# Performance work log

Hardware: AMD Instinct MI355X
Metric: run time of the kernel (lower is better)

## Reference

```python
import jax, jax.numpy as jnp
import numpy as np
import math

E = 512; V = 8192; B = 32; T = 16; L = 4; FF = 2048; NH = 8; TEMP = 1.0


def setup_inputs() -> dict:
    key = jax.random.key(0)
    ks = jax.random.split(key, 16)
    s = 0.02
    nrm = lambda k, shape, sc=s: jax.random.normal(k, shape, jnp.float32) * sc
    d = {}
    d['encoder_state'] = nrm(ks[0], (1, B, E), 1.0)
    d['special_symbol'] = nrm(ks[1], (1, 1, E))
    d['embed_weight'] = nrm(ks[2], (V, E), E ** -0.5)
    d['out_w'] = nrm(ks[3], (V, E))
    d['out_b'] = jnp.zeros((V,), jnp.float32)
    u = jax.random.uniform(ks[4], (T, B, V), jnp.float32, 1e-6, 1.0 - 1e-6)
    d['gumbel'] = -jnp.log(-jnp.log(u))
    d['sa_qkv_w'] = nrm(ks[5], (L, 3 * E, E)); d['sa_qkv_b'] = jnp.zeros((L, 3 * E), jnp.float32)
    d['sa_out_w'] = nrm(ks[6], (L, E, E)); d['sa_out_b'] = jnp.zeros((L, E), jnp.float32)
    d['ca_qkv_w'] = nrm(ks[7], (L, 3 * E, E)); d['ca_qkv_b'] = jnp.zeros((L, 3 * E), jnp.float32)
    d['ca_out_w'] = nrm(ks[8], (L, E, E)); d['ca_out_b'] = jnp.zeros((L, E), jnp.float32)
    for i in (1, 2, 3):
        d['ln%d_g' % i] = jnp.ones((L, E), jnp.float32)
        d['ln%d_b' % i] = jnp.zeros((L, E), jnp.float32)
    d['w1'] = nrm(ks[9], (L, FF, E)); d['b1'] = jnp.zeros((L, FF), jnp.float32)
    d['w2'] = nrm(ks[10], (L, E, FF)); d['b2'] = jnp.zeros((L, E), jnp.float32)
    return d


def _ln(x, g, b):
    m = x.mean(-1, keepdims=True)
    v = ((x - m) ** 2).mean(-1, keepdims=True)
    return (x - m) / jnp.sqrt(v + 1e-5) * g + b


def _mha(q_in, kv_in, qkv_w, qkv_b, out_w, out_b, mask):
    # q_in: [Sq,B,E], kv_in: [Sk,B,E]; fused PyTorch-style in_proj
    hd = E // NH
    wq, wk, wv = jnp.split(qkv_w, 3, 0)
    bq, bk, bv = jnp.split(qkv_b, 3, 0)
    q = (q_in @ wq.T + bq).reshape(q_in.shape[0], -1, NH, hd)
    k = (kv_in @ wk.T + bk).reshape(kv_in.shape[0], -1, NH, hd)
    v = (kv_in @ wv.T + bv).reshape(kv_in.shape[0], -1, NH, hd)
    s = jnp.einsum('qbhd,kbhd->bhqk', q, k) / math.sqrt(hd)
    if mask is not None:
        s = s + mask
    a = jax.nn.softmax(s, -1)
    o = jnp.einsum('bhqk,kbhd->qbhd', a, v).reshape(q_in.shape[0], -1, E)
    return o @ out_w.T + out_b


def _forward(encoder_state, special_symbol, embed_weight, out_w, out_b, gumbel,
             sa_qkv_w, sa_qkv_b, sa_out_w, sa_out_b,
             ca_qkv_w, ca_qkv_b, ca_out_w, ca_out_b,
             ln1_g, ln1_b, ln2_g, ln2_b, ln3_g, ln3_b,
             w1, b1, w2, b2):
    bsz = encoder_state.shape[1]
    embed_scale = math.sqrt(E)
    inp = jnp.broadcast_to(special_symbol, (1, bsz, E))  # special start symbol
    seq_steps, distribs = [], []
    for step in range(T):
        t = step + 1
        mask = jnp.where(jnp.triu(jnp.ones((t, t), bool), 1), -jnp.inf, 0.0)
        x = inp
        for l in range(L):  # post-norm TransformerDecoderLayer, erf-gelu
            sa = _mha(x, x, sa_qkv_w[l], sa_qkv_b[l], sa_out_w[l], sa_out_b[l], mask)
            x = _ln(x + sa, ln1_g[l], ln1_b[l])
            ca = _mha(x, encoder_state, ca_qkv_w[l], ca_qkv_b[l], ca_out_w[l], ca_out_b[l], None)
            x = _ln(x + ca, ln2_g[l], ln2_b[l])
            ff = jax.nn.gelu(x @ w1[l].T + b1[l], approximate=False) @ w2[l].T + b2[l]
            x = _ln(x + ff, ln3_g[l], ln3_b[l])
        logits = x[-1] @ out_w.T + out_b  # [B,V], last position only
        distribs.append(jax.nn.softmax(logits, -1))
        sample = jax.nn.softmax((logits + gumbel[step]) / TEMP, -1)  # gumbel-softmax (training mode)
        seq_steps.append(sample)
        new_emb = (sample @ embed_weight) * embed_scale  # soft embedding lookup
        inp = jnp.concatenate([inp, new_emb[None]], 0)
    sequence = jnp.stack(seq_steps).transpose(1, 0, 2)  # [B,T,V]
    eos = jnp.zeros_like(sequence[:, :1, :]).at[:, :, 0].set(1.0)
    sequence = jnp.concatenate([sequence, eos], 1)  # [B,T+1,V]
    return sequence, jnp.stack(distribs)  # distribs: [T,B,V]


def reference(encoder_state, special_symbol, embed_weight, out_w, out_b, gumbel,
              sa_qkv_w, sa_qkv_b, sa_out_w, sa_out_b,
              ca_qkv_w, ca_qkv_b, ca_out_w, ca_out_b,
              ln1_g, ln1_b, ln2_g, ln2_b, ln3_g, ln3_b,
              w1, b1, w2, b2):
    return _forward(encoder_state, special_symbol, embed_weight, out_w, out_b, gumbel,
                    sa_qkv_w, sa_qkv_b, sa_out_w, sa_out_b,
                    ca_qkv_w, ca_qkv_b, ca_out_w, ca_out_b,
                    ln1_g, ln1_b, ln2_g, ln2_b, ln3_g, ln3_b,
                    w1, b1, w2, b2)
```

## Files before the change

kernel.cpp:

```cpp
#include <hip/hip_runtime.h>
#include <math.h>

#define BB 32
#define EE 512
#define VV 8192
#define TT 16
#define LL 4
#define FFD 2048
#define NHD 8
#define HDD 64
#define LDP 520
#define RWP 516
#define OLP 72
#define SCALE_EMB 22.627416997969522f

typedef __attribute__((ext_vector_type(8))) short bf16x8;
typedef __attribute__((ext_vector_type(4))) float f32x4;
typedef unsigned long long ull;

__device__ __forceinline__ f32x4 mfma16(bf16x8 a, bf16x8 b, f32x4 c){
  return __builtin_amdgcn_mfma_f32_16x16x32_bf16(a, b, c, 0, 0, 0);
}

__device__ __forceinline__ float wave_sum(float v){
  for (int o = 32; o; o >>= 1) v += __shfl_down(v, o);
  return __shfl(v, 0);
}
__device__ __forceinline__ unsigned short f_to_bf(float f){
  unsigned u = __float_as_uint(f);
  unsigned r = (u + 0x7fffu + ((u >> 16) & 1u)) >> 16;
  return (unsigned short)r;
}
__device__ __forceinline__ float2 bf2_to_f2(const unsigned short* p){
  unsigned u = *(const unsigned*)p;
  float2 r;
  r.x = __uint_as_float(u << 16);
  r.y = __uint_as_float(u & 0xffff0000u);
  return r;
}
union UF { ull u; unsigned short s[4]; };
__device__ __forceinline__ ull pkbf4(float a, float b, float c, float d){
  UF x; x.s[0] = f_to_bf(a); x.s[1] = f_to_bf(b); x.s[2] = f_to_bf(c); x.s[3] = f_to_bf(d); return x.u;
}

__device__ __forceinline__ void gemm_chunk(const float* __restrict__ wrow0, int ldw,
    const unsigned short* xs, float* wt, float acc[4][2]){
  const int t = threadIdx.x, fg = t & 15, bg = t >> 4;
  #pragma unroll 1
  for (int c = 0; c < 8; ++c){
    const int k0 = c*64;
    __syncthreads();
    {
      int i = t*4;
      #pragma unroll
      for (int p = 0; p < 4; ++p, i += 1024){
        const int fr = i >> 6, kk = i & 63;
        float4 v = *(const float4*)(wrow0 + (size_t)fr*ldw + k0 + kk);
        wt[(kk+0)*68 + fr] = v.x;
        wt[(kk+1)*68 + fr] = v.y;
        wt[(kk+2)*68 + fr] = v.z;
        wt[(kk+3)*68 + fr] = v.w;
      }
    }
    __syncthreads();
    const unsigned short* xr0 = xs + (bg*2)*EE + k0;
    const unsigned short* xr1 = xr0 + EE;
    #pragma unroll 8
    for (int k = 0; k < 64; k += 2){
      float w0[4], w1[4];
      *(float4*)w0 = *(const float4*)(wt + (k+0)*68 + fg*4);
      *(float4*)w1 = *(const float4*)(wt + (k+1)*68 + fg*4);
      float2 xv0 = bf2_to_f2(xr0 + k);
      float2 xv1 = bf2_to_f2(xr1 + k);
      #pragma unroll
      for (int i = 0; i < 4; ++i){
        acc[i][0] += w0[i]*xv0.x + w1[i]*xv0.y;
        acc[i][1] += w0[i]*xv1.x + w1[i]*xv1.y;
      }
    }
  }
}

__device__ __forceinline__ void stage_x_512(unsigned short* xs,
    const float* __restrict__ xraw, const float* __restrict__ ybuf,
    const float* __restrict__ g, const float* __restrict__ bt, int use_ln,
    float* __restrict__ xlnout){
  if (!use_ln){
    for (int i = threadIdx.x*4; i < BB*EE; i += 2048){
      float4 v = *(const float4*)(xraw + i);
      int r = i >> 9, c = i & 511;
      *(ull*)(xs + r*LDP + c) = pkbf4(v.x, v.y, v.z, v.w);
    }
  } else {
    const int lane = threadIdx.x & 63, wv = threadIdx.x >> 6;
    for (int r = wv*4; r < wv*4 + 4; ++r){
      float vals[8]; float s = 0.f, s2 = 0.f;
      #pragma unroll
      for (int j = 0; j < 8; ++j){
        float v = ybuf[r*EE + lane + j*64];
        vals[j] = v; s += v; s2 += v*v;
      }
      s = wave_sum(s); s2 = wave_sum(s2);
      float m = s * (1.f/EE);
      float inv = rsqrtf(s2*(1.f/EE) - m*m + 1e-5f);
      #pragma unroll
      for (int j = 0; j < 8; ++j){
        int c = lane + j*64;
        float v = (vals[j]-m)*inv*g[c] + bt[c];
        xs[r*LDP + c] = f_to_bf(v);
        if (xlnout) xlnout[r*EE + c] = v;
      }
    }
  }
  __syncthreads();
}


__global__ __launch_bounds__(256) void k_init(const float* __restrict__ special,
    float* __restrict__ dseq, float* __restrict__ x,
    float* __restrict__ o2a, float* __restrict__ o2b,
    float* __restrict__ y0, float* __restrict__ y1){
  int idx = blockIdx.x*256 + threadIdx.x;
  if (idx < BB*VV){
    int b = idx >> 13, v = idx & (VV-1);
    dseq[(size_t)b*((TT+1)*VV) + (size_t)TT*VV + v] = (v == 0) ? 1.f : 0.f;
  } else if (idx < BB*VV + BB*EE){
    x[idx - BB*VV] = special[idx & (EE-1)];
  } else if (idx < BB*VV + 2*BB*EE){
    o2a[idx - BB*VV - BB*EE] = 0.f;
  } else if (idx < BB*VV + 3*BB*EE){
    o2b[idx - BB*VV - 2*BB*EE] = 0.f;
  } else if (idx < BB*VV + 4*BB*EE){
    y0[idx - BB*VV - 3*BB*EE] = 0.f;
  } else if (idx < BB*VV + 5*BB*EE){
    y1[idx - BB*VV - 4*BB*EE] = 0.f;
  }
}

__global__ __launch_bounds__(256) void k_penc(const float* __restrict__ enc,
    const float* __restrict__ w, const float* __restrict__ bias, float* __restrict__ venc){
  __shared__ unsigned short xs[BB*EE];
  __shared__ float wt[64*68];
  const int l = blockIdx.x >> 3, et = blockIdx.x & 7;
  for (int i = threadIdx.x; i < BB*EE; i += 256) xs[i] = f_to_bf(enc[i]);
  const int t = threadIdx.x, fg = t & 15, bg = t >> 4;
  const int f0 = et*64;
  const float* wl = w + (size_t)l*3*EE*EE + (size_t)(2*EE + f0)*EE;
  const float* bl = bias + l*3*EE + 2*EE + f0;
  float acc[4][2];
  #pragma unroll
  for (int i = 0; i < 4; ++i){ float bv = bl[fg*4+i]; acc[i][0] = bv; acc[i][1] = bv; }
  gemm_chunk(wl, EE, xs, wt, acc);
  #pragma unroll
  for (int i = 0; i < 4; ++i)
    #pragma unroll
    for (int j = 0; j < 2; ++j)
      venc[(size_t)l*BB*EE + (bg*2+j)*EE + f0 + fg*4 + i] = acc[i][j];
}

__global__ __launch_bounds__(256) void k_pca(const float* __restrict__ venc,
    const float* __restrict__ w, const float* __restrict__ bias, float* __restrict__ cac){
  __shared__ unsigned short xs[BB*EE];
  __shared__ float wt[64*68];
  const int l = blockIdx.x >> 3, et = blockIdx.x & 7;
  const float* vin = venc + (size_t)l*BB*EE;
  for (int i = threadIdx.x; i < BB*EE; i += 256) xs[i] = f_to_bf(vin[i]);
  const int t = threadIdx.x, fg = t & 15, bg = t >> 4;
  const int f0 = et*64;
  const float* wl = w + (size_t)l*EE*EE + (size_t)f0*EE;
  const float* bl = bias + l*EE + f0;
  float acc[4][2];
  #pragma unroll
  for (int i = 0; i < 4; ++i){ float bv = bl[fg*4+i]; acc[i][0] = bv; acc[i][1] = bv; }
  gemm_chunk(wl, EE, xs, wt, acc);
  #pragma unroll
  for (int i = 0; i < 4; ++i)
    #pragma unroll
    for (int j = 0; j < 2; ++j)
      cac[(size_t)l*BB*EE + (bg*2+j)*EE + f0 + fg*4 + i] = acc[i][j];
}

__global__ __launch_bounds__(256) void k_cvt(const float* __restrict__ s,
    unsigned short* __restrict__ d, int n4){
  int i = blockIdx.x*256 + threadIdx.x;
  if (i < n4){
    float4 v = ((const float4*)s)[i];
    ushort4 o;
    o.x = f_to_bf(v.x); o.y = f_to_bf(v.y); o.z = f_to_bf(v.z); o.w = f_to_bf(v.w);
    ((ushort4*)d)[i] = o;
  }
}

__global__ __launch_bounds__(256) void k_embT(const float* __restrict__ emb,
    unsigned short* __restrict__ eT){
  __shared__ unsigned short tl[64][68];
  const int vt = blockIdx.x >> 3, et = blockIdx.x & 7;
  const int v0 = vt*64, e0 = et*64;
  for (int i = threadIdx.x; i < 64*64; i += 256){
    int vv = i >> 6, ee = i & 63;
    tl[vv][ee] = f_to_bf(emb[(size_t)(v0+vv)*EE + e0 + ee]);
  }
  __syncthreads();
  for (int i = threadIdx.x; i < 64*64; i += 256){
    int ee = i >> 6, vv = i & 63;
    eT[(size_t)(e0+ee)*VV + v0 + vv] = tl[vv][ee];
  }
}


__global__ __launch_bounds__(512) void k_A(
    const float* __restrict__ x, const float* __restrict__ ybuf,
    const float* __restrict__ lng, const float* __restrict__ lnb, int use_ln,
    const unsigned short* __restrict__ Wb, const float* __restrict__ bias,
    const unsigned short* __restrict__ owb_l,
    float* __restrict__ kcl, float* __restrict__ vcl,
    float* __restrict__ xln, float* __restrict__ o2,
    float* __restrict__ gs, int tpos, int tlen){
  __shared__ unsigned short xs[BB*LDP];
  __shared__ __align__(16) float qs[BB*68];
  __shared__ float att[BB*16];
  const int h = blockIdx.x;
  const int t = threadIdx.x;
  if (!use_ln && h == 0 && t < 64) gs[t] = 0.f;
  stage_x_512(xs, x, ybuf, lng, lnb, use_ln, (use_ln && h == 0) ? xln : nullptr);
  const int wv = t >> 6, lane = t & 63;
  const int lm = lane & 15, kg = lane >> 4;
  const unsigned short* b0r = xs + lm*LDP + kg*8;
  const unsigned short* b1r = xs + (lm+16)*LDP + kg*8;
  if (wv < 6){
    const int c = wv >> 1, half = wv & 1;
    #pragma unroll
    for (int ft = 0; ft < 2; ++ft){
      const int frel_t = (half*2 + ft)*16;
      const unsigned short* ar = Wb + (size_t)(c*EE + h*64 + frel_t + lm)*EE + kg*8;
      f32x4 acc0 = {0.f,0.f,0.f,0.f}, acc1 = {0.f,0.f,0.f,0.f};
      #pragma unroll 4
      for (int ks = 0; ks < 16; ++ks){
        bf16x8 a  = *reinterpret_cast<const bf16x8*>(ar + ks*32);
        bf16x8 b0 = *reinterpret_cast<const bf16x8*>(b0r + ks*32);
        bf16x8 b1 = *reinterpret_cast<const bf16x8*>(b1r + ks*32);
        acc0 = mfma16(a, b0, acc0);
        acc1 = mfma16(a, b1, acc1);
      }
      #pragma unroll
      for (int r = 0; r < 4; ++r){
        const int frel = frel_t + kg*4 + r;
        const float bv = bias[c*EE + h*64 + frel];
        float v0 = acc0[r] + bv, v1 = acc1[r] + bv;
        if (c == 0){
          qs[lm*68 + frel] = v0;
          qs[(lm+16)*68 + frel] = v1;
        } else if (c == 1){
          kcl[((lm*NHD + h)*TT + tpos)*HDD + frel] = v0;
          kcl[(((lm+16)*NHD + h)*TT + tpos)*HDD + frel] = v1;
        } else {
          vcl[((lm*NHD + h)*TT + tpos)*HDD + frel] = v0;
          vcl[(((lm+16)*NHD + h)*TT + tpos)*HDD + frel] = v1;
        }
      }
    }
  }
  __syncthreads();
  {
    const int b = t >> 4, j = t & 15;
    if (j < tlen){
      const float* qrow = qs + b*68;
      const float* krow = kcl + ((b*NHD + h)*TT + j)*HDD;
      float a = 0.f;
      #pragma unroll
      for (int d = 0; d < HDD; d += 4){
        float4 qv = *(const float4*)(qrow + d);
        float4 kv = *(const float4*)(krow + d);
        a += qv.x*kv.x + qv.y*kv.y + qv.z*kv.z + qv.w*kv.w;
      }
      att[b*16 + j] = a*0.125f;
    }
  }
  __syncthreads();
  if (t < 32){
    const int b = t;
    float m = -1e30f;
    for (int j = 0; j < tlen; ++j) m = fmaxf(m, att[b*16 + j]);
    float s = 0.f;
    for (int j = 0; j < tlen; ++j) s += __expf(att[b*16 + j] - m);
    float inv = 1.f/s;
    for (int j = 0; j < tlen; ++j) att[b*16 + j] = __expf(att[b*16 + j] - m)*inv;
  }
  __syncthreads();
  unsigned short* o_lds = (unsigned short*)qs;
  {
    const int b = t >> 4, d0 = (t & 15)*4;
    float acc[4];
    #pragma unroll
    for (int i = 0; i < 4; ++i) acc[i] = 0.f;
    const float* vrow = vcl + ((b*NHD + h)*TT)*HDD + d0;
    for (int j = 0; j < tlen; ++j){
      const float a = att[b*16 + j];
      float4 v = *(const float4*)(vrow + j*HDD);
      acc[0] += a*v.x; acc[1] += a*v.y; acc[2] += a*v.z; acc[3] += a*v.w;
    }
    *(ull*)(o_lds + b*OLP + d0) = pkbf4(acc[0], acc[1], acc[2], acc[3]);
  }
  __syncthreads();
  const unsigned short* ob0 = o_lds + lm*OLP + kg*8;
  const unsigned short* ob1 = o_lds + (lm+16)*OLP + kg*8;
  #pragma unroll
  for (int ft = 0; ft < 4; ++ft){
    const int f0 = wv*64 + ft*16;
    const unsigned short* ar = owb_l + (size_t)(f0 + lm)*EE + h*HDD + kg*8;
    f32x4 a0 = {0.f,0.f,0.f,0.f}, a1 = {0.f,0.f,0.f,0.f};
    #pragma unroll
    for (int ks = 0; ks < 2; ++ks){
      bf16x8 a  = *reinterpret_cast<const bf16x8*>(ar + ks*32);
      bf16x8 x0 = *reinterpret_cast<const bf16x8*>(ob0 + ks*32);
      bf16x8 x1 = *reinterpret_cast<const bf16x8*>(ob1 + ks*32);
      a0 = mfma16(a, x0, a0);
      a1 = mfma16(a, x1, a1);
    }
    #pragma unroll
    for (int r = 0; r < 4; ++r){
      const int f = f0 + kg*4 + r;
      atomicAdd(&o2[lm*EE + f], a0[r]);
      atomicAdd(&o2[(lm+16)*EE + f], a1[r]);
    }
  }
}

__global__ __launch_bounds__(512) void k_BC(
    const float* __restrict__ o2buf, const float* __restrict__ resid,
    const float* __restrict__ ob, const float* __restrict__ cac,
    const float* __restrict__ g1, const float* __restrict__ b1g,
    const float* __restrict__ g2, const float* __restrict__ b2g,
    const float* __restrict__ b2bias,
    const unsigned short* __restrict__ w1b, const float* __restrict__ b1bias,
    const unsigned short* __restrict__ w2b,
    float* __restrict__ ycur, float* __restrict__ yzero, float* __restrict__ o2zero,
    float* __restrict__ xz){
  __shared__ unsigned short xs[BB*LDP];
  __shared__ __align__(16) float rawf[BB*RWP];
  __shared__ unsigned short Hs[BB*OLP];
  const int t = threadIdx.x, blk = blockIdx.x;
  for (int i = t*4; i < BB*EE; i += 2048){
    const int r = i >> 9, c = i & 511;
    float4 a  = *(const float4*)(o2buf + i);
    float4 rr = *(const float4*)(resid + i);
    float4 ov = *(const float4*)(ob + c);
    rawf[r*RWP + c]     = a.x + rr.x + ov.x;
    rawf[r*RWP + c + 1] = a.y + rr.y + ov.y;
    rawf[r*RWP + c + 2] = a.z + rr.z + ov.z;
    rawf[r*RWP + c + 3] = a.w + rr.w + ov.w;
  }
  __syncthreads();
  const int wv = t >> 6, lane = t & 63;
  const int lm = lane & 15, kg = lane >> 4;
  {
    const int c0 = lane*4, c1 = 256 + lane*4;
    for (int r = wv*4; r < wv*4 + 4; ++r){
      float v[8];
      *(float4*)(v+0) = *(const float4*)(rawf + r*RWP + c0);
      *(float4*)(v+4) = *(const float4*)(rawf + r*RWP + c1);
      float s = 0.f, s2 = 0.f;
      #pragma unroll
      for (int j = 0; j < 8; ++j){ s += v[j]; s2 += v[j]*v[j]; }
      s = wave_sum(s); s2 = wave_sum(s2);
      float m = s*(1.f/EE), inv = rsqrtf(s2*(1.f/EE) - m*m + 1e-5f);
      float4 ca0 = *(const float4*)(cac + (size_t)r*EE + c0);
      float4 ca1 = *(const float4*)(cac + (size_t)r*EE + c1);
      float nv[8]; float u = 0.f, u2 = 0.f;
      nv[0] = (v[0]-m)*inv*g1[c0+0] + b1g[c0+0] + ca0.x;
      nv[1] = (v[1]-m)*inv*g1[c0+1] + b1g[c0+1] + ca0.y;
      nv[2] = (v[2]-m)*inv*g1[c0+2] + b1g[c0+2] + ca0.z;
      nv[3] = (v[3]-m)*inv*g1[c0+3] + b1g[c0+3] + ca0.w;
      nv[4] = (v[4]-m)*inv*g1[c1+0] + b1g[c1+0] + ca1.x;
      nv[5] = (v[5]-m)*inv*g1[c1+1] + b1g[c1+1] + ca1.y;
      nv[6] = (v[6]-m)*inv*g1[c1+2] + b1g[c1+2] + ca1.z;
      nv[7] = (v[7]-m)*inv*g1[c1+3] + b1g[c1+3] + ca1.w;
      #pragma unroll
      for (int j = 0; j < 8; ++j){ u += nv[j]; u2 += nv[j]*nv[j]; }
      u = wave_sum(u); u2 = wave_sum(u2);
      float m2 = u*(1.f/EE), inv2 = rsqrtf(u2*(1.f/EE) - m2*m2 + 1e-5f);
      float o0 = (nv[0]-m2)*inv2*g2[c0+0] + b2g[c0+0];
      float o1 = (nv[1]-m2)*inv2*g2[c0+1] + b2g[c0+1];
      float o2v = (nv[2]-m2)*inv2*g2[c0+2] + b2g[c0+2];
      float o3 = (nv[3]-m2)*inv2*g2[c0+3] + b2g[c0+3];
      float o4 = (nv[4]-m2)*inv2*g2[c1+0] + b2g[c1+0];
      float o5 = (nv[5]-m2)*inv2*g2[c1+1] + b2g[c1+1];
      float o6 = (nv[6]-m2)*inv2*g2[c1+2] + b2g[c1+2];
      float o7 = (nv[7]-m2)*inv2*g2[c1+3] + b2g[c1+3];
      *(ull*)(xs + r*LDP + c0) = pkbf4(o0, o1, o2v, o3);
      *(ull*)(xs + r*LDP + c1) = pkbf4(o4, o5, o6, o7);
      if ((c0 >> 4) == blk){
        atomicAdd(&ycur[(size_t)r*EE + c0+0], o0 + b2bias[c0+0]);
        atomicAdd(&ycur[(size_t)r*EE + c0+1], o1 + b2bias[c0+1]);
        atomicAdd(&ycur[(size_t)r*EE + c0+2], o2v + b2bias[c0+2]);
        atomicAdd(&ycur[(size_t)r*EE + c0+3], o3 + b2bias[c0+3]);
      }
      if ((c1 >> 4) == blk){
        atomicAdd(&ycur[(size_t)r*EE + c1+0], o4 + b2bias[c1+0]);
        atomicAdd(&ycur[(size_t)r*EE + c1+1], o5 + b2bias[c1+1]);
        atomicAdd(&ycur[(size_t)r*EE + c1+2], o6 + b2bias[c1+2]);
        atomicAdd(&ycur[(size_t)r*EE + c1+3], o7 + b2bias[c1+3]);
      }
    }
  }
  __syncthreads();
  {
    const int ftile = wv & 3, rh = wv >> 2;
    const int f0w = blk*64 + ftile*16;
    const unsigned short* ar = w1b + (size_t)(f0w + lm)*EE + kg*8;
    const unsigned short* br = xs + (lm + rh*16)*LDP + kg*8;
    f32x4 acc = {0.f,0.f,0.f,0.f};
    #pragma unroll 4
    for (int ks = 0; ks < 16; ++ks){
      bf16x8 a = *reinterpret_cast<const bf16x8*>(ar + ks*32);
      bf16x8 b = *reinterpret_cast<const bf16x8*>(br + ks*32);
      acc = mfma16(a, b, acc);
    }
    const int fbrel = ftile*16 + kg*4;
    float hh[4];
    #pragma unroll
    for (int r = 0; r < 4; ++r){
      const float bv = b1bias[blk*64 + fbrel + r];
      float vv = acc[r] + bv;
      hh[r] = 0.5f*vv*(1.f + erff(vv*0.70710678118654752f));
    }
    *(ull*)(Hs + (lm + rh*16)*OLP + fbrel) = pkbf4(hh[0], hh[1], hh[2], hh[3]);
  }
  __syncthreads();
  {
    const unsigned short* hb0 = Hs + lm*OLP + kg*8;
    const unsigned short* hb1 = Hs + (lm+16)*OLP + kg*8;
    #pragma unroll
    for (int et = 0; et < 4; ++et){
      const int e0 = (wv*4 + et)*16;
      const unsigned short* ar = w2b + (size_t)(e0 + lm)*FFD + blk*64 + kg*8;
      f32x4 a0 = {0.f,0.f,0.f,0.f}, a1 = {0.f,0.f,0.f,0.f};
      #pragma unroll
      for (int ks = 0; ks < 2; ++ks){
        bf16x8 a  = *reinterpret_cast<const bf16x8*>(ar + ks*32);
        bf16x8 h0 = *reinterpret_cast<const bf16x8*>(hb0 + ks*32);
        bf16x8 h1 = *reinterpret_cast<const bf16x8*>(hb1 + ks*32);
        a0 = mfma16(a, h0, a0);
        a1 = mfma16(a, h1, a1);
      }
      #pragma unroll
      for (int r = 0; r < 4; ++r){
        const int e = e0 + kg*4 + r;
        atomicAdd(&ycur[lm*EE + e], a0[r]);
        atomicAdd(&ycur[(lm+16)*EE + e], a1[r]);
      }
    }
  }
  yzero[blk*512 + t] = 0.f;
  o2zero[blk*512 + t] = 0.f;
  if (xz) xz[blk*512 + t] = 0.f;
}

__global__ __launch_bounds__(512) void k_logits_e(
    const float* __restrict__ ybuf, const float* __restrict__ lng, const float* __restrict__ lnb,
    const unsigned short* __restrict__ Wb, const float* __restrict__ bias,
    const float* __restrict__ gum,
    float* __restrict__ el, float* __restrict__ eg, float* __restrict__ gs){
  __shared__ unsigned short xs[BB*LDP];
  __shared__ float ls[64];
  const int t = threadIdx.x;
  if (t < 64) ls[t] = 0.f;
  stage_x_512(xs, nullptr, ybuf, lng, lnb, 1, nullptr);
  const int wv = t >> 6, lane = t & 63;
  const int lm = lane & 15, kg = lane >> 4;
  const int ftile = wv & 3, rh = wv >> 2;
  const int f0w = blockIdx.x*64 + ftile*16;
  const int b = lm + rh*16;
  const unsigned short* ar = Wb + (size_t)(f0w + lm)*EE + kg*8;
  const unsigned short* br = xs + b*LDP + kg*8;
  f32x4 acc = {0.f,0.f,0.f,0.f};
  #pragma unroll 4
  for (int ks = 0; ks < 16; ++ks){
    bf16x8 a = *reinterpret_cast<const bf16x8*>(ar + ks*32);
    bf16x8 bb = *reinterpret_cast<const bf16x8*>(br + ks*32);
    acc = mfma16(a, bb, acc);
  }
  const int fb = f0w + kg*4;
  float4 g4 = *(const float4*)(gum + (size_t)b*VV + fb);
  float l0 = acc[0] + bias[fb+0], l1 = acc[1] + bias[fb+1];
  float l2 = acc[2] + bias[fb+2], l3 = acc[3] + bias[fb+3];
  float e10 = __expf(l0), e11 = __expf(l1), e12 = __expf(l2), e13 = __expf(l3);
  float e20 = __expf(l0+g4.x), e21 = __expf(l1+g4.y), e22 = __expf(l2+g4.z), e23 = __expf(l3+g4.w);
  float4 ev1; ev1.x=e10; ev1.y=e11; ev1.z=e12; ev1.w=e13;
  float4 ev2; ev2.x=e20; ev2.y=e21; ev2.z=e22; ev2.w=e23;
  *(float4*)(el + (size_t)b*VV + fb) = ev1;
  *(float4*)(eg + (size_t)b*VV + fb) = ev2;
  atomicAdd(&ls[b],      e10+e11+e12+e13);
  atomicAdd(&ls[32 + b], e20+e21+e22+e23);
  __syncthreads();
  if (t < 64) atomicAdd(&gs[t], ls[t]);
}

__global__ __launch_bounds__(512) void k_SMEM(
    const unsigned short* __restrict__ eT,
    const float* __restrict__ el, const float* __restrict__ eg,
    const float* __restrict__ gs,
    float* __restrict__ dseq, float* __restrict__ ddist,
    float* __restrict__ x, int step){
  __shared__ unsigned short ss[BB*LDP];
  __shared__ float rr[64];
  const int t = threadIdx.x;
  const int et = blockIdx.x & 7, v0 = (blockIdx.x >> 3)*512;
  if (t < 64) rr[t] = 1.f / gs[t];
  __syncthreads();
  for (int i = t*4; i < BB*512; i += 2048){
    const int r = i >> 9, c = i & 511;
    float4 e4 = *(const float4*)(eg + (size_t)r*VV + v0 + c);
    const float r2v = rr[32 + r];
    *(ull*)(ss + r*LDP + c) = pkbf4(e4.x*r2v, e4.y*r2v, e4.z*r2v, e4.w*r2v);
  }
  __syncthreads();
  const int wv = t >> 6, lane = t & 63;
  const int lm = lane & 15, kg = lane >> 4;
  const int etile = wv & 3, rh = wv >> 2;
  const int e0 = et*64 + etile*16;
  const unsigned short* ar = eT + (size_t)(e0 + lm)*VV + v0 + kg*8;
  const unsigned short* br = ss + (lm + rh*16)*LDP + kg*8;
  f32x4 acc = {0.f,0.f,0.f,0.f};
  #pragma unroll 4
  for (int ks = 0; ks < 16; ++ks){
    bf16x8 a = *reinterpret_cast<const bf16x8*>(ar + ks*32);
    bf16x8 b = *reinterpret_cast<const bf16x8*>(br + ks*32);
    acc = mfma16(a, b, acc);
  }
  #pragma unroll
  for (int r = 0; r < 4; ++r){
    const int e = e0 + kg*4 + r;
    atomicAdd(&x[(lm + rh*16)*EE + e], acc[r]*SCALE_EMB);
  }
  if (et == 0){
    for (int i = t*4; i < BB*512; i += 2048){
      const int r = i >> 9, c = i & 511;
      float4 e2 = *(const float4*)(eg + (size_t)r*VV + v0 + c);
      float4 e1 = *(const float4*)(el + (size_t)r*VV + v0 + c);
      const float r1v = rr[r], r2v = rr[32 + r];
      float4 dq; dq.x=e2.x*r2v; dq.y=e2.y*r2v; dq.z=e2.z*r2v; dq.w=e2.w*r2v;
      float4 dd; dd.x=e1.x*r1v; dd.y=e1.y*r1v; dd.z=e1.z*r1v; dd.w=e1.w*r1v;
      *(float4*)(dseq + (size_t)r*((TT+1)*VV) + (size_t)step*VV + v0 + c) = dq;
      *(float4*)(ddist + (size_t)r*VV + v0 + c) = dd;
    }
  }
}

extern "C" void kernel_launch(void* const* d_in, const int* in_sizes, int n_in,
                              void* d_out, int out_size, void* d_ws, size_t ws_size,
                              hipStream_t stream){
  (void)in_sizes; (void)n_in; (void)out_size; (void)ws_size;
  const float* enc  = (const float*)d_in[0];
  const float* spec = (const float*)d_in[1];
  const float* embw = (const float*)d_in[2];
  const float* outw = (const float*)d_in[3];
  const float* outb = (const float*)d_in[4];
  const float* gumb = (const float*)d_in[5];
  const float* saqw = (const float*)d_in[6];
  const float* saqb = (const float*)d_in[7];
  const float* saow = (const float*)d_in[8];
  const float* saob = (const float*)d_in[9];
  const float* caqw = (const float*)d_in[10];
  const float* caqb = (const float*)d_in[11];
  const float* caow = (const float*)d_in[12];
  const float* caob = (const float*)d_in[13];
  const float* l1g  = (const float*)d_in[14];
  const float* l1b  = (const float*)d_in[15];
  const float* l2g  = (const float*)d_in[16];
  const float* l2b  = (const float*)d_in[17];
  const float* l3g  = (const float*)d_in[18];
  const float* l3b  = (const float*)d_in[19];
  const float* w1   = (const float*)d_in[20];
  const float* b1   = (const float*)d_in[21];
  const float* w2   = (const float*)d_in[22];
  const float* b2   = (const float*)d_in[23];

  float* dout = (float*)d_out;
  float* dseq = dout;
  float* ddistbase = dout + (size_t)BB*(TT+1)*VV;

  unsigned char* p = (unsigned char*)d_ws;
  auto alloc = [&](size_t bytes) -> void* {
    void* r = (void*)p; p += (bytes + 255) & ~(size_t)255; return r;
  };
  float* x      = (float*)alloc(BB*EE*4);
  float* y0     = (float*)alloc(BB*EE*4);
  float* y1     = (float*)alloc(BB*EE*4);
  float* xln    = (float*)alloc(BB*EE*4);
  float* o2a    = (float*)alloc(BB*EE*4);
  float* o2b    = (float*)alloc(BB*EE*4);
  float* el     = (float*)alloc((size_t)BB*VV*4);
  float* eg     = (float*)alloc((size_t)BB*VV*4);
  float* gs     = (float*)alloc(64*4);
  float* venc   = (float*)alloc((size_t)LL*BB*EE*4);
  float* cac    = (float*)alloc((size_t)LL*BB*EE*4);
  float* kcache = (float*)alloc((size_t)LL*BB*EE*TT*4);
  float* vcache = (float*)alloc((size_t)LL*BB*EE*TT*4);
  unsigned short* wqkvb = (unsigned short*)alloc((size_t)LL*3*EE*EE*2);
  unsigned short* owb   = (unsigned short*)alloc((size_t)LL*EE*EE*2);
  unsigned short* w1b   = (unsigned short*)alloc((size_t)LL*FFD*EE*2);
  unsigned short* w2b   = (unsigned short*)alloc((size_t)LL*FFD*EE*2);
  unsigned short* outwb = (unsigned short*)alloc((size_t)VV*EE*2);
  unsigned short* eTb   = (unsigned short*)alloc((size_t)EE*VV*2);

  k_init<<<1344, 256, 0, stream>>>(spec, dseq, x, o2a, o2b, y0, y1);
  k_penc<<<32, 256, 0, stream>>>(enc, caqw, caqb, venc);
  k_pca<<<32, 256, 0, stream>>>(venc, caow, caob, cac);
  k_cvt<<<(LL*3*EE*EE/4 + 255)/256, 256, 0, stream>>>(saqw, wqkvb, LL*3*EE*EE/4);
  k_cvt<<<(LL*EE*EE/4 + 255)/256, 256, 0, stream>>>(saow, owb, LL*EE*EE/4);
  k_cvt<<<(LL*FFD*EE/4 + 255)/256, 256, 0, stream>>>(w1, w1b, LL*FFD*EE/4);
  k_cvt<<<(LL*FFD*EE/4 + 255)/256, 256, 0, stream>>>(w2, w2b, LL*FFD*EE/4);
  k_cvt<<<(VV*EE/4 + 255)/256, 256, 0, stream>>>(outw, outwb, VV*EE/4);
  k_embT<<<1024, 256, 0, stream>>>(embw, eTb);

  float* yb[2]  = { y0, y1 };
  float* o2p[2] = { o2a, o2b };

  for (int step = 0; step < TT; ++step){
    const int tpos = step, tlen = step + 1;
    for (int l = 0; l < LL; ++l){
      const int use_ln = (l > 0);
      const int par = l & 1, opp = par ^ 1;
      const float* lg = l3g + (use_ln ? (l-1)*EE : 0);
      const float* lb = l3b + (use_ln ? (l-1)*EE : 0);
      float* kcl = kcache + (size_t)l*BB*EE*TT;
      float* vcl = vcache + (size_t)l*BB*EE*TT;
      k_A<<<NHD, 512, 0, stream>>>(x, yb[opp], lg, lb, use_ln,
          wqkvb + (size_t)l*3*EE*EE, saqb + (size_t)l*3*EE,
          owb + (size_t)l*EE*EE, kcl, vcl, xln, o2p[par], gs, tpos, tlen);
      k_BC<<<32, 512, 0, stream>>>(o2p[par], use_ln ? xln : x,
          saob + (size_t)l*EE, cac + (size_t)l*BB*EE,
          l1g + l*EE, l1b + l*EE, l2g + l*EE, l2b + l*EE, b2 + l*EE,
          w1b + (size_t)l*FFD*EE, b1 + l*FFD, w2b + (size_t)l*EE*FFD,
          yb[par], yb[opp], o2p[opp], (l == 1) ? x : nullptr);
    }
    k_logits_e<<<128, 512, 0, stream>>>(yb[1], l3g + 3*EE, l3b + 3*EE, outwb, outb,
        gumb + (size_t)step*BB*VV, el, eg, gs);
    k_SMEM<<<128, 512, 0, stream>>>(eTb, el, eg, gs, dseq,
        ddistbase + (size_t)step*BB*VV, x, step);
  }
}
```

Baseline: 4.163 ms.

## Split attention, logits and soft-embedding kernels across more, smaller blocks

k_A now splits each head's work over two batch halves, giving 16 blocks instead of 8, with staging and LDS sized for 16 rows. k_logits_e and k_SMEM move to 256 blocks of 256 threads, with narrower vocabulary tiles per block, to fill more of the GPU's compute units. The cost is that weight tiles are loaded twice as often across blocks, the logits kernel repeats the LayerNorm staging per block, and more atomics hit the accumulators.

```diff
diff --git a/kernel.cpp b/kernel.cpp
--- a/kernel.cpp
+++ b/kernel.cpp
@@ -12,6 +12,7 @@
 #define LDP 520
 #define RWP 516
 #define OLP 72
+#define SSP 264
 #define SCALE_EMB 22.627416997969522f
 
 typedef __attribute__((ext_vector_type(8))) short bf16x8;
@@ -81,23 +82,24 @@
   }
 }
 
-__device__ __forceinline__ void stage_x_512(unsigned short* xs,
+__device__ __forceinline__ void stage_half_512(unsigned short* xs, int rb,
     const float* __restrict__ xraw, const float* __restrict__ ybuf,
     const float* __restrict__ g, const float* __restrict__ bt, int use_ln,
     float* __restrict__ xlnout){
   if (!use_ln){
-    for (int i = threadIdx.x*4; i < BB*EE; i += 2048){
-      float4 v = *(const float4*)(xraw + i);
+    for (int i = threadIdx.x*4; i < 16*EE; i += 2048){
+      float4 v = *(const float4*)(xraw + (size_t)rb*EE + i);
       int r = i >> 9, c = i & 511;
       *(ull*)(xs + r*LDP + c) = pkbf4(v.x, v.y, v.z, v.w);
     }
   } else {
     const int lane = threadIdx.x & 63, wv = threadIdx.x >> 6;
-    for (int r = wv*4; r < wv*4 + 4; ++r){
+    for (int r = wv*2; r < wv*2 + 2; ++r){
+      const float* yr = ybuf + (size_t)(rb + r)*EE;
       float vals[8]; float s = 0.f, s2 = 0.f;
       #pragma unroll
       for (int j = 0; j < 8; ++j){
-        float v = ybuf[r*EE + lane + j*64];
+        float v = yr[lane + j*64];
         vals[j] = v; s += v; s2 += v*v;
       }
       s = wave_sum(s); s2 = wave_sum(s2);
@@ -108,8 +110,31 @@
         int c = lane + j*64;
         float v = (vals[j]-m)*inv*g[c] + bt[c];
         xs[r*LDP + c] = f_to_bf(v);
-        if (xlnout) xlnout[r*EE + c] = v;
-      }
+        if (xlnout) xlnout[(size_t)(rb + r)*EE + c] = v;
+      }
+    }
+  }
+  __syncthreads();
+}
+
+__device__ __forceinline__ void stage_ln_256(unsigned short* xs,
+    const float* __restrict__ ybuf, const float* __restrict__ g,
+    const float* __restrict__ bt){
+  const int lane = threadIdx.x & 63, wv = threadIdx.x >> 6;
+  for (int r = wv*8; r < wv*8 + 8; ++r){
+    float vals[8]; float s = 0.f, s2 = 0.f;
+    #pragma unroll
+    for (int j = 0; j < 8; ++j){
+      float v = ybuf[(size_t)r*EE + lane + j*64];
+      vals[j] = v; s += v; s2 += v*v;
+    }
+    s = wave_sum(s); s2 = wave_sum(s2);
+    float m = s * (1.f/EE);
+    float inv = rsqrtf(s2*(1.f/EE) - m*m + 1e-5f);
+    #pragma unroll
+    for (int j = 0; j < 8; ++j){
+      int c = lane + j*64;
+      xs[r*LDP + c] = f_to_bf((vals[j]-m)*inv*g[c] + bt[c]);
     }
   }
   __syncthreads();
@@ -216,56 +241,49 @@
     float* __restrict__ kcl, float* __restrict__ vcl,
     float* __restrict__ xln, float* __restrict__ o2,
     float* __restrict__ gs, int tpos, int tlen){
-  __shared__ unsigned short xs[BB*LDP];
-  __shared__ __align__(16) float qs[BB*68];
-  __shared__ float att[BB*16];
-  const int h = blockIdx.x;
+  __shared__ unsigned short xs[16*LDP];
+  __shared__ __align__(16) float qs[16*68];
+  __shared__ float att[16*16];
+  const int h = blockIdx.x >> 1, bh = blockIdx.x & 1, rb = bh*16;
   const int t = threadIdx.x;
-  if (!use_ln && h == 0 && t < 64) gs[t] = 0.f;
-  stage_x_512(xs, x, ybuf, lng, lnb, use_ln, (use_ln && h == 0) ? xln : nullptr);
+  if (!use_ln && blockIdx.x == 0 && t < 64) gs[t] = 0.f;
+  stage_half_512(xs, rb, x, ybuf, lng, lnb, use_ln, (use_ln && h == 0) ? xln : nullptr);
   const int wv = t >> 6, lane = t & 63;
   const int lm = lane & 15, kg = lane >> 4;
-  const unsigned short* b0r = xs + lm*LDP + kg*8;
-  const unsigned short* b1r = xs + (lm+16)*LDP + kg*8;
+  const unsigned short* br = xs + lm*LDP + kg*8;
   if (wv < 6){
     const int c = wv >> 1, half = wv & 1;
     #pragma unroll
     for (int ft = 0; ft < 2; ++ft){
       const int frel_t = (half*2 + ft)*16;
       const unsigned short* ar = Wb + (size_t)(c*EE + h*64 + frel_t + lm)*EE + kg*8;
-      f32x4 acc0 = {0.f,0.f,0.f,0.f}, acc1 = {0.f,0.f,0.f,0.f};
+      f32x4 acc = {0.f,0.f,0.f,0.f};
       #pragma unroll 4
       for (int ks = 0; ks < 16; ++ks){
-        bf16x8 a  = *reinterpret_cast<const bf16x8*>(ar + ks*32);
-        bf16x8 b0 = *reinterpret_cast<const bf16x8*>(b0r + ks*32);
-        bf16x8 b1 = *reinterpret_cast<const bf16x8*>(b1r + ks*32);
-        acc0 = mfma16(a, b0, acc0);
-        acc1 = mfma16(a, b1, acc1);
+        bf16x8 a = *reinterpret_cast<const bf16x8*>(ar + ks*32);
+        bf16x8 b = *reinterpret_cast<const bf16x8*>(br + ks*32);
+        acc = mfma16(a, b, acc);
       }
       #pragma unroll
       for (int r = 0; r < 4; ++r){
         const int frel = frel_t + kg*4 + r;
-        const float bv = bias[c*EE + h*64 + frel];
-        float v0 = acc0[r] + bv, v1 = acc1[r] + bv;
+        const float v0 = acc[r] + bias[c*EE + h*64 + frel];
         if (c == 0){
           qs[lm*68 + frel] = v0;
-          qs[(lm+16)*68 + frel] = v1;
         } else if (c == 1){
-          kcl[((lm*NHD + h)*TT + tpos)*HDD + frel] = v0;
-          kcl[(((lm+16)*NHD + h)*TT + tpos)*HDD + frel] = v1;
+          kcl[(((rb+lm)*NHD + h)*TT + tpos)*HDD + frel] = v0;
         } else {
-          vcl[((lm*NHD + h)*TT + tpos)*HDD + frel] = v0;
-          vcl[(((lm+16)*NHD + h)*TT + tpos)*HDD + frel] = v1;
+          vcl[(((rb+lm)*NHD + h)*TT + tpos)*HDD + frel] = v0;
         }
       }
     }
   }
   __syncthreads();
-  {
-    const int b = t >> 4, j = t & 15;
+  if (t < 256){
+    const int bl = t >> 4, j = t & 15;
     if (j < tlen){
-      const float* qrow = qs + b*68;
-      const float* krow = kcl + ((b*NHD + h)*TT + j)*HDD;
+      const float* qrow = qs + bl*68;
+      const float* krow = kcl + (((rb+bl)*NHD + h)*TT + j)*HDD;
       float a = 0.f;
       #pragma unroll
       for (int d = 0; d < HDD; d += 4){
@@ -273,55 +291,51 @@
         float4 kv = *(const float4*)(krow + d);
         a += qv.x*kv.x + qv.y*kv.y + qv.z*kv.z + qv.w*kv.w;
       }
-      att[b*16 + j] = a*0.125f;
-    }
-  }
-  __syncthreads();
-  if (t < 32){
-    const int b = t;
+      att[bl*16 + j] = a*0.125f;
+    }
+  }
+  __syncthreads();
+  if (t < 16){
+    const int bl = t;
     float m = -1e30f;
-    for (int j = 0; j < tlen; ++j) m = fmaxf(m, att[b*16 + j]);
+    for (int j = 0; j < tlen; ++j) m = fmaxf(m, att[bl*16 + j]);
     float s = 0.f;
-    for (int j = 0; j < tlen; ++j) s += __expf(att[b*16 + j] - m);
+    for (int j = 0; j < tlen; ++j) s += __expf(att[bl*16 + j] - m);
     float inv = 1.f/s;
-    for (int j = 0; j < tlen; ++j) att[b*16 + j] = __expf(att[b*16 + j] - m)*inv;
+    for (int j = 0; j < tlen; ++j) att[bl*16 + j] = __expf(att[bl*16 + j] - m)*inv;
   }
   __syncthreads();
   unsigned short* o_lds = (unsigned short*)qs;
-  {
-    const int b = t >> 4, d0 = (t & 15)*4;
+  if (t < 256){
+    const int bl = t >> 4, d0 = (t & 15)*4;
     float acc[4];
     #pragma unroll
     for (int i = 0; i < 4; ++i) acc[i] = 0.f;
-    const float* vrow = vcl + ((b*NHD + h)*TT)*HDD + d0;
+    const float* vrow = vcl + (((rb+bl)*NHD + h)*TT)*HDD + d0;
     for (int j = 0; j < tlen; ++j){
-      const float a = att[b*16 + j];
+      const float a = att[bl*16 + j];
       float4 v = *(const float4*)(vrow + j*HDD);
       acc[0] += a*v.x; acc[1] += a*v.y; acc[2] += a*v.z; acc[3] += a*v.w;
     }
-    *(ull*)(o_lds + b*OLP + d0) = pkbf4(acc[0], acc[1], acc[2], acc[3]);
-  }
-  __syncthreads();
-  const unsigned short* ob0 = o_lds + lm*OLP + kg*8;
-  const unsigned short* ob1 = o_lds + (lm+16)*OLP + kg*8;
+    *(ull*)(o_lds + bl*OLP + d0) = pkbf4(acc[0], acc[1], acc[2], acc[3]);
+  }
+  __syncthreads();
+  const unsigned short* ob = o_lds + lm*OLP + kg*8;
   #pragma unroll
   for (int ft = 0; ft < 4; ++ft){
     const int f0 = wv*64 + ft*16;
     const unsigned short* ar = owb_l + (size_t)(f0 + lm)*EE + h*HDD + kg*8;
-    f32x4 a0 = {0.f,0.f,0.f,0.f}, a1 = {0.f,0.f,0.f,0.f};
+    f32x4 a0 = {0.f,0.f,0.f,0.f};
     #pragma unroll
     for (int ks = 0; ks < 2; ++ks){
       bf16x8 a  = *reinterpret_cast<const bf16x8*>(ar + ks*32);
-      bf16x8 x0 = *reinterpret_cast<const bf16x8*>(ob0 + ks*32);
-      bf16x8 x1 = *reinterpret_cast<const bf16x8*>(ob1 + ks*32);
+      bf16x8 x0 = *reinterpret_cast<const bf16x8*>(ob + ks*32);
       a0 = mfma16(a, x0, a0);
-      a1 = mfma16(a, x1, a1);
     }
     #pragma unroll
     for (int r = 0; r < 4; ++r){
       const int f = f0 + kg*4 + r;
-      atomicAdd(&o2[lm*EE + f], a0[r]);
-      atomicAdd(&o2[(lm+16)*EE + f], a1[r]);
+      atomicAdd(&o2[(rb+lm)*EE + f], a0[r]);
     }
   }
 }
@@ -456,7 +470,7 @@
   if (xz) xz[blk*512 + t] = 0.f;
 }
 
-__global__ __launch_bounds__(512) void k_logits_e(
+__global__ __launch_bounds__(256) void k_logits_e(
     const float* __restrict__ ybuf, const float* __restrict__ lng, const float* __restrict__ lnb,
     const unsigned short* __restrict__ Wb, const float* __restrict__ bias,
     const float* __restrict__ gum,
@@ -465,11 +479,11 @@
   __shared__ float ls[64];
   const int t = threadIdx.x;
   if (t < 64) ls[t] = 0.f;
-  stage_x_512(xs, nullptr, ybuf, lng, lnb, 1, nullptr);
+  stage_ln_256(xs, ybuf, lng, lnb);
   const int wv = t >> 6, lane = t & 63;
   const int lm = lane & 15, kg = lane >> 4;
-  const int ftile = wv & 3, rh = wv >> 2;
-  const int f0w = blockIdx.x*64 + ftile*16;
+  const int ftile = wv & 1, rh = wv >> 1;
+  const int f0w = blockIdx.x*32 + ftile*16;
   const int b = lm + rh*16;
   const unsigned short* ar = Wb + (size_t)(f0w + lm)*EE + kg*8;
   const unsigned short* br = xs + b*LDP + kg*8;
@@ -496,46 +510,50 @@
   if (t < 64) atomicAdd(&gs[t], ls[t]);
 }
 
-__global__ __launch_bounds__(512) void k_SMEM(
+__global__ __launch_bounds__(256) void k_SMEM(
     const unsigned short* __restrict__ eT,
     const float* __restrict__ el, const float* __restrict__ eg,
     const float* __restrict__ gs,
     float* __restrict__ dseq, float* __restrict__ ddist,
     float* __restrict__ x, int step){
-  __shared__ unsigned short ss[BB*LDP];
+  __shared__ unsigned short ss[BB*SSP];
   __shared__ float rr[64];
   const int t = threadIdx.x;
-  const int et = blockIdx.x & 7, v0 = (blockIdx.x >> 3)*512;
+  const int et = blockIdx.x & 7, v0 = (blockIdx.x >> 3)*256;
   if (t < 64) rr[t] = 1.f / gs[t];
   __syncthreads();
-  for (int i = t*4; i < BB*512; i += 2048){
-    const int r = i >> 9, c = i & 511;
+  for (int i = t*4; i < BB*256; i += 1024){
+    const int r = i >> 8, c = i & 255;
     float4 e4 = *(const float4*)(eg + (size_t)r*VV + v0 + c);
     const float r2v = rr[32 + r];
-    *(ull*)(ss + r*LDP + c) = pkbf4(e4.x*r2v, e4.y*r2v, e4.z*r2v, e4.w*r2v);
+    *(ull*)(ss + r*SSP + c) = pkbf4(e4.x*r2v, e4.y*r2v, e4.z*r2v, e4.w*r2v);
   }
   __syncthreads();
   const int wv = t >> 6, lane = t & 63;
   const int lm = lane & 15, kg = lane >> 4;
-  const int etile = wv & 3, rh = wv >> 2;
-  const int e0 = et*64 + etile*16;
-  const unsigned short* ar = eT + (size_t)(e0 + lm)*VV + v0 + kg*8;
-  const unsigned short* br = ss + (lm + rh*16)*LDP + kg*8;
-  f32x4 acc = {0.f,0.f,0.f,0.f};
-  #pragma unroll 4
-  for (int ks = 0; ks < 16; ++ks){
-    bf16x8 a = *reinterpret_cast<const bf16x8*>(ar + ks*32);
-    bf16x8 b = *reinterpret_cast<const bf16x8*>(br + ks*32);
-    acc = mfma16(a, b, acc);
-  }
+  const int rh = wv >> 1;
+  const unsigned short* br = ss + (lm + rh*16)*SSP + kg*8;
   #pragma unroll
-  for (int r = 0; r < 4; ++r){
-    const int e = e0 + kg*4 + r;
-    atomicAdd(&x[(lm + rh*16)*EE + e], acc[r]*SCALE_EMB);
+  for (int ft = 0; ft < 2; ++ft){
+    const int etile = (wv & 1)*2 + ft;
+    const int e0 = et*64 + etile*16;
+    const unsigned short* ar = eT + (size_t)(e0 + lm)*VV + v0 + kg*8;
+    f32x4 acc = {0.f,0.f,0.f,0.f};
+    #pragma unroll 4
+    for (int ks = 0; ks < 8; ++ks){
+      bf16x8 a = *reinterpret_cast<const bf16x8*>(ar + ks*32);
+      bf16x8 b = *reinterpret_cast<const bf16x8*>(br + ks*32);
+      acc = mfma16(a, b, acc);
+    }
+    #pragma unroll
+    for (int r = 0; r < 4; ++r){
+      const int e = e0 + kg*4 + r;
+      atomicAdd(&x[(lm + rh*16)*EE + e], acc[r]*SCALE_EMB);
+    }
   }
   if (et == 0){
-    for (int i = t*4; i < BB*512; i += 2048){
-      const int r = i >> 9, c = i & 511;
+    for (int i = t*4; i < BB*256; i += 1024){
+      const int r = i >> 8, c = i & 255;
       float4 e2 = *(const float4*)(eg + (size_t)r*VV + v0 + c);
       float4 e1 = *(const float4*)(el + (size_t)r*VV + v0 + c);
       const float r1v = rr[r], r2v = rr[32 + r];
@@ -626,7 +644,7 @@
       const float* lb = l3b + (use_ln ? (l-1)*EE : 0);
       float* kcl = kcache + (size_t)l*BB*EE*TT;
       float* vcl = vcache + (size_t)l*BB*EE*TT;
-      k_A<<<NHD, 512, 0, stream>>>(x, yb[opp], lg, lb, use_ln,
+      k_A<<<16, 512, 0, stream>>>(x, yb[opp], lg, lb, use_ln,
           wqkvb + (size_t)l*3*EE*EE, saqb + (size_t)l*3*EE,
           owb + (size_t)l*EE*EE, kcl, vcl, xln, o2p[par], gs, tpos, tlen);
       k_BC<<<32, 512, 0, stream>>>(o2p[par], use_ln ? xln : x,
@@ -635,9 +653,9 @@
           w1b + (size_t)l*FFD*EE, b1 + l*FFD, w2b + (size_t)l*EE*FFD,
           yb[par], yb[opp], o2p[opp], (l == 1) ? x : nullptr);
     }
-    k_logits_e<<<128, 512, 0, stream>>>(yb[1], l3g + 3*EE, l3b + 3*EE, outwb, outb,
+    k_logits_e<<<256, 256, 0, stream>>>(yb[1], l3g + 3*EE, l3b + 3*EE, outwb, outb,
         gumb + (size_t)step*BB*VV, el, eg, gs);
-    k_SMEM<<<128, 512, 0, stream>>>(eTb, el, eg, gs, dseq,
+    k_SMEM<<<256, 256, 0, stream>>>(eTb, el, eg, gs, dseq,
         ddistbase + (size_t)step*BB*VV, x, step);
   }
 }
```

Result: faster. 3.827 ms (-8.1%).
